# Kernel tuning notes

Hardware: AMD Instinct MI355X
Metric: run time of the kernel (lower is better)

The kernel has to match this reference:

```python
import jax, jax.numpy as jnp
import numpy as np

B, N, K, H = 8, 256, 64, 768
NUM_CLASSES = 10
D_SIM = 0.3  # self.d in the torch module


def setup_inputs() -> dict:
    key = jax.random.key(0)
    ks = jax.random.split(key, 12)
    s = 0.02  # init scale to keep 3 stacked linear GCN layers numerically tame
    return {
        "encoder_out": jax.random.normal(ks[0], (B, N, H), jnp.float32),
        "landmarks": jax.random.normal(ks[1], (K, H), jnp.float32),
        "alpha": jnp.array([0.5], jnp.float32),
        "gcn_w1": jax.random.normal(ks[2], (H, H), jnp.float32) * s,
        "gcn_b1": jnp.zeros((H,), jnp.float32),
        "gcn_w2": jax.random.normal(ks[3], (H, H), jnp.float32) * s,
        "gcn_b2": jnp.zeros((H,), jnp.float32),
        "gcn_w3": jax.random.normal(ks[4], (H, H), jnp.float32) * s,
        "gcn_b3": jnp.zeros((H,), jnp.float32),
        "fc1_w": jax.random.normal(ks[5], (1000, K * H), jnp.float32) * s,
        "fc1_b": jnp.zeros((1000,), jnp.float32),
        "fc2_w": jax.random.normal(ks[6], (100, 1000), jnp.float32) * s,
        "fc2_b": jnp.zeros((100,), jnp.float32),
        "fc3_w": jax.random.normal(ks[7], (NUM_CLASSES, 100), jnp.float32) * s,
        "fc3_b": jnp.zeros((NUM_CLASSES,), jnp.float32),
    }


def reference(encoder_out, landmarks, alpha,
              gcn_w1, gcn_b1, gcn_w2, gcn_b2, gcn_w3, gcn_b3,
              fc1_w, fc1_b, fc2_w, fc2_b, fc3_w, fc3_b):
    b, n, h = encoder_out.shape
    k = landmarks.shape[0]

    # distance_matrix: [B,N,K], min-max normalized over clusters
    diff = encoder_out[:, :, None, :] - landmarks[None, None, :, :]  # [B,N,K,H]
    dist = jnp.sqrt(jnp.sum(diff * diff, axis=-1))                   # [B,N,K]
    mn = dist.min(axis=-1, keepdims=True)
    mx = dist.max(axis=-1, keepdims=True)
    nd = (dist - mn) / (mx - mn + 1e-6)

    # probability_matrix: gaussian similarity, row-normalized
    sim = jnp.exp(-nd * nd / (2.0 * D_SIM * D_SIM))
    prob = sim / sim.sum(axis=-1, keepdims=True)  # [B,N,K]

    # compute_distance_weight: [N,N] smooth matrix
    idx = jnp.arange(n)
    dw = jnp.exp(-alpha[0] * jnp.abs(idx[:, None] - idx[None, :]).astype(jnp.float32))

    # graph_constructing: einsum('bik,bjl->bijkl') * W then sum over (k,l)
    # == bilinear form P @ W @ P^T, computed WITHOUT the 5-D tensor
    P = prob.transpose(0, 2, 1)                      # [B,K,N]
    G = jnp.einsum('bik,kl,bjl->bij', P, dw, P)      # [B,K,K]

    # cluster pooling: prob^T @ encoder_out -> [B,K,H]
    out = jnp.einsum('bnk,bnh->bkh', prob, encoder_out)
    out_ori = out  # dropout is identity at inference

    # gcn_batched: PyG GCNConv x3 on the dense graph G!=0, batched.
    # gcn_norm: add remaining self-loops, A_hat = A + I_missing,
    # out = D^-1/2 A_hat D^-1/2 (X W^T) + bias  (no nonlinearity between layers)
    A = (G != 0).astype(jnp.float32)                 # [B,K,K]
    A = jnp.maximum(A, jnp.eye(k, dtype=jnp.float32))
    deg = A.sum(axis=-1)                             # [B,K]
    dinv = jnp.where(deg > 0, 1.0 / jnp.sqrt(deg), 0.0)
    An = A * dinv[:, :, None] * dinv[:, None, :]     # normalized adjacency

    hx = out
    for w, bias in ((gcn_w1, gcn_b1), (gcn_w2, gcn_b2), (gcn_w3, gcn_b3)):
        hx = jnp.einsum('bij,bjh->bih', An, hx @ w.T) + bias
    gcn_out = hx + out  # residual inside gcn_batched

    x = (out_ori + gcn_out).reshape(b, -1)           # [B, K*H]
    x = jax.nn.gelu(x @ fc1_w.T + fc1_b, approximate=False)
    x = jax.nn.gelu(x @ fc2_w.T + fc2_b, approximate=False)
    return x @ fc3_w.T + fc3_b                       # [B, NUM_CLASSES]
```

## Files before the change

### kernel.cpp

```cpp
#include <hip/hip_runtime.h>
#include <math.h>

#define DEV __device__ __forceinline__

DEV float dot4(float4 a, float4 b){ return a.x*b.x + a.y*b.y + a.z*b.z + a.w*b.w; }

DEV float wave_sum(float v){
  #pragma unroll
  for (int off = 32; off; off >>= 1) v += __shfl_xor(v, off, 64);
  return v;
}

DEV float gelu_exact(float v){ return 0.5f * v * (1.f + erff(v * 0.70710678118654752f)); }

__global__ void k_lmT(const float* __restrict__ lm, float* __restrict__ lmT4,
                      float* __restrict__ lnorm){
  int k = blockIdx.x, t = threadIdx.x;
  __shared__ float red[256];
  float s = 0.f;
  if (t < 192){
    float4 v = *(const float4*)(lm + k*768 + 4*t);
    ((float4*)lmT4)[t*64 + k] = v;
    s = dot4(v, v);
  }
  red[t] = s; __syncthreads();
  for (int off = 128; off; off >>= 1){ if (t < off) red[t] += red[t+off]; __syncthreads(); }
  if (t == 0) lnorm[k] = red[0];
}

__global__ void k_prob(const float* __restrict__ enc, const float* __restrict__ lmT4,
                       const float* __restrict__ lnorm, float* __restrict__ prob){
  int t = threadIdx.x, lane = t & 63, wv = t >> 6;
  int row0 = blockIdx.x*8 + wv*2;
  const float4* LT = (const float4*)lmT4;
  const float4* X0 = (const float4*)(enc + (size_t)row0*768);
  const float4* X1 = (const float4*)(enc + (size_t)(row0+1)*768);
  float dot0=0.f, dot1=0.f, xn0=0.f, xn1=0.f;
  #pragma unroll 8
  for (int hg = 0; hg < 192; ++hg){
    float4 l4 = LT[hg*64 + lane];
    float4 a = X0[hg], b = X1[hg];
    dot0 += dot4(a, l4); dot1 += dot4(b, l4);
    xn0  += dot4(a, a);  xn1  += dot4(b, b);
  }
  float ln = lnorm[lane];
  float d0 = sqrtf(fmaxf(xn0 + ln - 2.f*dot0, 0.f));
  float d1 = sqrtf(fmaxf(xn1 + ln - 2.f*dot1, 0.f));
  float mn0=d0, mx0=d0, mn1=d1, mx1=d1;
  #pragma unroll
  for (int off = 32; off; off >>= 1){
    mn0 = fminf(mn0, __shfl_xor(mn0, off, 64));
    mx0 = fmaxf(mx0, __shfl_xor(mx0, off, 64));
    mn1 = fminf(mn1, __shfl_xor(mn1, off, 64));
    mx1 = fmaxf(mx1, __shfl_xor(mx1, off, 64));
  }
  float nd0 = (d0 - mn0) / (mx0 - mn0 + 1e-6f);
  float nd1 = (d1 - mn1) / (mx1 - mn1 + 1e-6f);
  float s0 = expf(nd0*nd0 * (-1.f/0.18f));
  float s1 = expf(nd1*nd1 * (-1.f/0.18f));
  float sum0 = wave_sum(s0), sum1 = wave_sum(s1);
  prob[(size_t)row0*64 + lane]     = s0 / sum0;
  prob[(size_t)(row0+1)*64 + lane] = s1 / sum1;
}

__global__ void k_pool(const float* __restrict__ enc, const float* __restrict__ prob,
                       float* __restrict__ outp, float* __restrict__ mbar){
  int b = blockIdx.x / 48, ch = blockIdx.x % 48;
  int lane = threadIdx.x & 63, wv = threadIdx.x >> 6;
  int h0 = ch*16 + wv*4;
  const float* E = enc + (size_t)b*256*768 + h0;
  const float* P = prob + (size_t)b*256*64;
  float acc[4] = {0,0,0,0};
  #pragma unroll 4
  for (int n = 0; n < 256; ++n){
    float p = P[n*64 + lane];
    float4 e0 = *(const float4*)(E + (size_t)n*768);
    acc[0] += p*e0.x; acc[1] += p*e0.y; acc[2] += p*e0.z; acc[3] += p*e0.w;
  }
  float* O = outp + ((size_t)b*64 + lane)*768 + h0;
  *(float4*)O = make_float4(acc[0],acc[1],acc[2],acc[3]);
  #pragma unroll
  for (int j = 0; j < 4; ++j){
    float v = wave_sum(acc[j]);
    if (lane == 0) mbar[(size_t)b*768 + h0 + j] = v * (1.f/64.f);
  }
}

__global__ void k_vm768(const float* __restrict__ in, const float* __restrict__ W,
                        const float* __restrict__ bias, float* __restrict__ out){
  int lane = threadIdx.x & 63, wv = threadIdx.x >> 6;
  int j = blockIdx.x*4 + wv;
  const float4* Wr = (const float4*)(W + (size_t)j*768);
  const float4* IN = (const float4*)in;
  float acc[8] = {0,0,0,0,0,0,0,0};
  #pragma unroll
  for (int s = 0; s < 3; ++s){
    int ig = s*64 + lane;
    float4 w4 = Wr[ig];
    #pragma unroll
    for (int b = 0; b < 8; ++b) acc[b] += dot4(w4, IN[b*192 + ig]);
  }
  #pragma unroll
  for (int b = 0; b < 8; ++b){
    float v = wave_sum(acc[b]);
    if (lane == 0) out[b*768 + j] = v + bias[j];
  }
}

__global__ void k_xcat(const float* __restrict__ outp, const float* __restrict__ hx3,
                       float* __restrict__ x){
  int idx = blockIdx.x*256 + threadIdx.x;
  int h4 = idx % 192;
  int b  = idx / (192*64);
  float4 o = ((const float4*)outp)[idx];
  float4 g = ((const float4*)hx3)[b*192 + h4];
  float4 r;
  r.x = 2.f*o.x + g.x; r.y = 2.f*o.y + g.y; r.z = 2.f*o.z + g.z; r.w = 2.f*o.w + g.w;
  ((float4*)x)[idx] = r;
}

__global__ void __launch_bounds__(256) k_fc1s(const float* __restrict__ x,
                                              const float* __restrict__ W,
                                              float* __restrict__ part_out){
  int t = threadIdx.x, lane = t & 63, wv = t >> 6;
  int kc = blockIdx.x / 125, jg = blockIdx.x % 125;
  int j0 = jg*8;
  const float4* Xg = (const float4*)x + kc*384;
  const float4* Wa = (const float4*)W + (size_t)(j0 + wv*2)*12288 + kc*384;
  const float4* Wb = Wa + 12288;
  __shared__ float4 xs4[3072];
  __shared__ float sp[64];

  float4 wa[6], wb[6];
  #pragma unroll
  for (int s = 0; s < 6; ++s){ wa[s] = Wa[s*64 + lane]; wb[s] = Wb[s*64 + lane]; }

  #pragma unroll
  for (int i = 0; i < 12; ++i){
    int idx = i*256 + t;
    int b = idx / 384, r = idx - b*384;
    xs4[idx] = Xg[b*12288 + r];
  }
  __syncthreads();

  float acc0[8] = {0,0,0,0,0,0,0,0};
  float acc1[8] = {0,0,0,0,0,0,0,0};
  #pragma unroll
  for (int s = 0; s < 6; ++s){
    int ig = s*64 + lane;
    #pragma unroll
    for (int b = 0; b < 8; ++b){
      float4 xv = xs4[b*384 + ig];
      acc0[b] += dot4(wa[s], xv);
      acc1[b] += dot4(wb[s], xv);
    }
  }

  #pragma unroll
  for (int b = 0; b < 8; ++b){
    float v0 = wave_sum(acc0[b]);
    float v1 = wave_sum(acc1[b]);
    if (lane == 0){ sp[(wv*2+0)*8 + b] = v0; sp[(wv*2+1)*8 + b] = v1; }
  }
  __syncthreads();
  if (t < 64)
    part_out[(size_t)kc*8000 + (size_t)j0*8 + t] = sp[t];
}

__global__ void k_fc1red(const float* __restrict__ part, const float* __restrict__ bias,
                         float* __restrict__ x1){
  int idx = blockIdx.x*256 + threadIdx.x;
  if (idx < 8000){
    int j = idx % 1000, b = idx / 1000;
    float v = 0.f;
    #pragma unroll
    for (int kc = 0; kc < 32; ++kc)
      v += part[kc*8000 + j*8 + b];
    x1[idx] = gelu_exact(v + bias[j]);
  }
}

__global__ void k_fc2(const float* __restrict__ x1, const float* __restrict__ W,
                      const float* __restrict__ bias, float* __restrict__ x2){
  int lane = threadIdx.x & 63, wv = threadIdx.x >> 6;
  int m = blockIdx.x*4 + wv;
  const float4* Wr = (const float4*)(W + (size_t)m*1000);
  const float4* X  = (const float4*)x1;
  float acc[8] = {0,0,0,0,0,0,0,0};
  for (int s = 0; s < 4; ++s){
    int jg = s*64 + lane;
    if (jg < 250){
      float4 w4 = Wr[jg];
      #pragma unroll
      for (int b = 0; b < 8; ++b) acc[b] += dot4(w4, X[b*250 + jg]);
    }
  }
  #pragma unroll
  for (int b = 0; b < 8; ++b){
    float v = wave_sum(acc[b]);
    if (lane == 0) x2[b*100 + m] = gelu_exact(v + bias[m]);
  }
}

__global__ void k_fc3(const float* __restrict__ x2, const float* __restrict__ W,
                      const float* __restrict__ bias, float* __restrict__ out){
  int t = threadIdx.x;
  if (t < 80){
    int b = t/10, c = t%10;
    float acc = bias[c];
    for (int m = 0; m < 100; ++m) acc += x2[b*100+m] * W[c*100+m];
    out[t] = acc;
  }
}

extern "C" void kernel_launch(void* const* d_in, const int* in_sizes, int n_in,
                              void* d_out, int out_size, void* d_ws, size_t ws_size,
                              hipStream_t stream){
  const float* enc = (const float*)d_in[0];
  const float* lm  = (const float*)d_in[1];
  const float* w1  = (const float*)d_in[3];
  const float* b1  = (const float*)d_in[4];
  const float* w2  = (const float*)d_in[5];
  const float* b2  = (const float*)d_in[6];
  const float* w3  = (const float*)d_in[7];
  const float* b3  = (const float*)d_in[8];
  const float* fw1 = (const float*)d_in[9];
  const float* fb1 = (const float*)d_in[10];
  const float* fw2 = (const float*)d_in[11];
  const float* fb2 = (const float*)d_in[12];
  const float* fw3 = (const float*)d_in[13];
  const float* fb3 = (const float*)d_in[14];

  float* ws    = (float*)d_ws;
  float* lmT4  = ws;
  float* lnorm = lmT4  + 49152;
  float* prob  = lnorm + 64;
  float* outp  = prob  + 131072;
  float* mbar  = outp  + 393216;
  float* hx1   = mbar  + 6144;
  float* hx2   = hx1   + 6144;
  float* hx3   = hx2   + 6144;
  float* xcat  = hx3   + 6144;
  float* fc1p  = xcat  + 393216;
  float* x1    = fc1p  + 256000;
  float* x2    = x1    + 8000;
  float* out   = (float*)d_out;

  k_lmT   <<<64,  256, 0, stream>>>(lm, lmT4, lnorm);
  k_prob  <<<256, 256, 0, stream>>>(enc, lmT4, lnorm, prob);
  k_pool  <<<384, 256, 0, stream>>>(enc, prob, outp, mbar);
  k_vm768 <<<192, 256, 0, stream>>>(mbar, w1, b1, hx1);
  k_vm768 <<<192, 256, 0, stream>>>(hx1,  w2, b2, hx2);
  k_vm768 <<<192, 256, 0, stream>>>(hx2,  w3, b3, hx3);
  k_xcat  <<<384, 256, 0, stream>>>(outp, hx3, xcat);
  k_fc1s  <<<4000,256, 0, stream>>>(xcat, fw1, fc1p);
  k_fc1red<<<32,  256, 0, stream>>>(fc1p, fb1, x1);
  k_fc2   <<<25,  256, 0, stream>>>(x1, fw2, fb2, x2);
  k_fc3   <<<1,   128, 0, stream>>>(x2, fw3, fb3, out);
}
```

Baseline: 144.6 us.

## Fuse landmark transpose, xcat, fc1 reduction and FC tail into fewer kernels

The landmark transpose and norm kernel is folded into k_prob, which now stages landmark chunks in shared memory and accumulates landmark norms in place. The xcat kernel is fused into the fc1 split-K kernel, which now uses half the K chunk and twice the blocks and reduces partials with atomicAdd into a buffer zeroed by k_prob. The fc1 reduction, fc2 and fc3 are merged into a single per-batch tail kernel. This removes several launches and the intermediate xcat and partial buffers, at the cost of atomic contention, redundant landmark norm work, and a nondeterministic summation order.

```diff
diff --git a/kernel.cpp b/kernel.cpp
--- a/kernel.cpp
+++ b/kernel.cpp
@@ -13,37 +13,37 @@
 
 DEV float gelu_exact(float v){ return 0.5f * v * (1.f + erff(v * 0.70710678118654752f)); }
 
-__global__ void k_lmT(const float* __restrict__ lm, float* __restrict__ lmT4,
-                      float* __restrict__ lnorm){
-  int k = blockIdx.x, t = threadIdx.x;
-  __shared__ float red[256];
-  float s = 0.f;
-  if (t < 192){
-    float4 v = *(const float4*)(lm + k*768 + 4*t);
-    ((float4*)lmT4)[t*64 + k] = v;
-    s = dot4(v, v);
-  }
-  red[t] = s; __syncthreads();
-  for (int off = 128; off; off >>= 1){ if (t < off) red[t] += red[t+off]; __syncthreads(); }
-  if (t == 0) lnorm[k] = red[0];
-}
-
-__global__ void k_prob(const float* __restrict__ enc, const float* __restrict__ lmT4,
-                       const float* __restrict__ lnorm, float* __restrict__ prob){
+__global__ void __launch_bounds__(256) k_prob(const float* __restrict__ lm,
+                                              const float* __restrict__ enc,
+                                              float* __restrict__ prob,
+                                              float* __restrict__ y1zero){
   int t = threadIdx.x, lane = t & 63, wv = t >> 6;
+  int gid = blockIdx.x*256 + t;
+  if (gid < 8000) y1zero[gid] = 0.f;
   int row0 = blockIdx.x*8 + wv*2;
-  const float4* LT = (const float4*)lmT4;
+  __shared__ float4 ls[3072];
+  const float4* L4 = (const float4*)lm;
   const float4* X0 = (const float4*)(enc + (size_t)row0*768);
-  const float4* X1 = (const float4*)(enc + (size_t)(row0+1)*768);
-  float dot0=0.f, dot1=0.f, xn0=0.f, xn1=0.f;
-  #pragma unroll 8
-  for (int hg = 0; hg < 192; ++hg){
-    float4 l4 = LT[hg*64 + lane];
-    float4 a = X0[hg], b = X1[hg];
-    dot0 += dot4(a, l4); dot1 += dot4(b, l4);
-    xn0  += dot4(a, a);  xn1  += dot4(b, b);
-  }
-  float ln = lnorm[lane];
+  const float4* X1 = X0 + 192;
+  float dot0=0.f, dot1=0.f, xn0=0.f, xn1=0.f, ln=0.f;
+  for (int c = 0; c < 4; ++c){
+    if (c) __syncthreads();
+    #pragma unroll
+    for (int i = 0; i < 12; ++i){
+      int idx = i*256 + t;
+      int k = idx & 63, col = idx >> 6;
+      ls[idx] = L4[k*192 + c*48 + col];
+    }
+    __syncthreads();
+    #pragma unroll 8
+    for (int hg = 0; hg < 48; ++hg){
+      float4 l4 = ls[hg*64 + lane];
+      float4 a = X0[c*48 + hg], b = X1[c*48 + hg];
+      dot0 += dot4(a, l4); dot1 += dot4(b, l4);
+      xn0  += dot4(a, a);  xn1  += dot4(b, b);
+      ln   += dot4(l4, l4);
+    }
+  }
   float d0 = sqrtf(fmaxf(xn0 + ln - 2.f*dot0, 0.f));
   float d1 = sqrtf(fmaxf(xn1 + ln - 2.f*dot1, 0.f));
   float mn0=d0, mx0=d0, mn1=d1, mx1=d1;
@@ -107,50 +107,44 @@
   }
 }
 
-__global__ void k_xcat(const float* __restrict__ outp, const float* __restrict__ hx3,
-                       float* __restrict__ x){
-  int idx = blockIdx.x*256 + threadIdx.x;
-  int h4 = idx % 192;
-  int b  = idx / (192*64);
-  float4 o = ((const float4*)outp)[idx];
-  float4 g = ((const float4*)hx3)[b*192 + h4];
-  float4 r;
-  r.x = 2.f*o.x + g.x; r.y = 2.f*o.y + g.y; r.z = 2.f*o.z + g.z; r.w = 2.f*o.w + g.w;
-  ((float4*)x)[idx] = r;
-}
-
-__global__ void __launch_bounds__(256) k_fc1s(const float* __restrict__ x,
+__global__ void __launch_bounds__(256) k_fc1s(const float* __restrict__ outp,
+                                              const float* __restrict__ hx3,
                                               const float* __restrict__ W,
-                                              float* __restrict__ part_out){
+                                              float* __restrict__ y1){
   int t = threadIdx.x, lane = t & 63, wv = t >> 6;
   int kc = blockIdx.x / 125, jg = blockIdx.x % 125;
   int j0 = jg*8;
-  const float4* Xg = (const float4*)x + kc*384;
-  const float4* Wa = (const float4*)W + (size_t)(j0 + wv*2)*12288 + kc*384;
+  const float4* O4 = (const float4*)outp + kc*192;
+  const float4* H4 = (const float4*)hx3;
+  const float4* Wa = (const float4*)W + (size_t)(j0 + wv*2)*12288 + kc*192;
   const float4* Wb = Wa + 12288;
-  __shared__ float4 xs4[3072];
+  __shared__ float4 xs4[1536];
   __shared__ float sp[64];
 
-  float4 wa[6], wb[6];
-  #pragma unroll
-  for (int s = 0; s < 6; ++s){ wa[s] = Wa[s*64 + lane]; wb[s] = Wb[s*64 + lane]; }
-
-  #pragma unroll
-  for (int i = 0; i < 12; ++i){
+  float4 wa[3], wb[3];
+  #pragma unroll
+  for (int s = 0; s < 3; ++s){ wa[s] = Wa[s*64 + lane]; wb[s] = Wb[s*64 + lane]; }
+
+  #pragma unroll
+  for (int i = 0; i < 6; ++i){
     int idx = i*256 + t;
-    int b = idx / 384, r = idx - b*384;
-    xs4[idx] = Xg[b*12288 + r];
+    int b = idx / 192, r = idx - b*192;
+    float4 o = O4[(size_t)b*12288 + r];
+    float4 g = H4[b*192 + r];
+    float4 v;
+    v.x = 2.f*o.x + g.x; v.y = 2.f*o.y + g.y; v.z = 2.f*o.z + g.z; v.w = 2.f*o.w + g.w;
+    xs4[idx] = v;
   }
   __syncthreads();
 
   float acc0[8] = {0,0,0,0,0,0,0,0};
   float acc1[8] = {0,0,0,0,0,0,0,0};
   #pragma unroll
-  for (int s = 0; s < 6; ++s){
+  for (int s = 0; s < 3; ++s){
     int ig = s*64 + lane;
     #pragma unroll
     for (int b = 0; b < 8; ++b){
-      float4 xv = xs4[b*384 + ig];
+      float4 xv = xs4[b*192 + ig];
       acc0[b] += dot4(wa[s], xv);
       acc1[b] += dot4(wb[s], xv);
     }
@@ -163,53 +157,48 @@
     if (lane == 0){ sp[(wv*2+0)*8 + b] = v0; sp[(wv*2+1)*8 + b] = v1; }
   }
   __syncthreads();
-  if (t < 64)
-    part_out[(size_t)kc*8000 + (size_t)j0*8 + t] = sp[t];
-}
-
-__global__ void k_fc1red(const float* __restrict__ part, const float* __restrict__ bias,
-                         float* __restrict__ x1){
-  int idx = blockIdx.x*256 + threadIdx.x;
-  if (idx < 8000){
-    int j = idx % 1000, b = idx / 1000;
-    float v = 0.f;
-    #pragma unroll
-    for (int kc = 0; kc < 32; ++kc)
-      v += part[kc*8000 + j*8 + b];
-    x1[idx] = gelu_exact(v + bias[j]);
-  }
-}
-
-__global__ void k_fc2(const float* __restrict__ x1, const float* __restrict__ W,
-                      const float* __restrict__ bias, float* __restrict__ x2){
-  int lane = threadIdx.x & 63, wv = threadIdx.x >> 6;
-  int m = blockIdx.x*4 + wv;
-  const float4* Wr = (const float4*)(W + (size_t)m*1000);
-  const float4* X  = (const float4*)x1;
-  float acc[8] = {0,0,0,0,0,0,0,0};
-  for (int s = 0; s < 4; ++s){
-    int jg = s*64 + lane;
-    if (jg < 250){
-      float4 w4 = Wr[jg];
-      #pragma unroll
-      for (int b = 0; b < 8; ++b) acc[b] += dot4(w4, X[b*250 + jg]);
-    }
-  }
-  #pragma unroll
-  for (int b = 0; b < 8; ++b){
-    float v = wave_sum(acc[b]);
-    if (lane == 0) x2[b*100 + m] = gelu_exact(v + bias[m]);
-  }
-}
-
-__global__ void k_fc3(const float* __restrict__ x2, const float* __restrict__ W,
-                      const float* __restrict__ bias, float* __restrict__ out){
-  int t = threadIdx.x;
-  if (t < 80){
-    int b = t/10, c = t%10;
-    float acc = bias[c];
-    for (int m = 0; m < 100; ++m) acc += x2[b*100+m] * W[c*100+m];
-    out[t] = acc;
+  if (t < 64){
+    int jp = t >> 3, b = t & 7;
+    atomicAdd(&y1[b*1000 + j0 + jp], sp[t]);
+  }
+}
+
+__global__ void __launch_bounds__(256) k_tail(const float* __restrict__ y1,
+                                              const float* __restrict__ fb1,
+                                              const float* __restrict__ W2,
+                                              const float* __restrict__ fb2,
+                                              const float* __restrict__ W3,
+                                              const float* __restrict__ fb3,
+                                              float* __restrict__ out){
+  int b = blockIdx.x, t = threadIdx.x, lane = t & 63, wv = t >> 6;
+  __shared__ __align__(16) float x1s[1000];
+  __shared__ float x2s[100];
+  #pragma unroll
+  for (int i = 0; i < 4; ++i){
+    int j = i*256 + t;
+    if (j < 1000) x1s[j] = gelu_exact(y1[b*1000 + j] + fb1[j]);
+  }
+  __syncthreads();
+  const float4* X4 = (const float4*)x1s;
+  for (int i = 0; i < 25; ++i){
+    int m = wv*25 + i;
+    const float4* Wr = (const float4*)(W2 + (size_t)m*1000);
+    float acc = 0.f;
+    #pragma unroll
+    for (int s = 0; s < 4; ++s){
+      int jg = s*64 + lane;
+      if (jg < 250) acc += dot4(Wr[jg], X4[jg]);
+    }
+    acc = wave_sum(acc);
+    if (lane == 0) x2s[m] = gelu_exact(acc + fb2[m]);
+  }
+  __syncthreads();
+  if (t < 10){
+    float acc = fb3[t];
+    const float* Wr = W3 + t*100;
+    #pragma unroll 4
+    for (int m = 0; m < 100; ++m) acc += x2s[m]*Wr[m];
+    out[b*10 + t] = acc;
   }
 }
 
@@ -232,29 +221,20 @@
   const float* fb3 = (const float*)d_in[14];
 
   float* ws    = (float*)d_ws;
-  float* lmT4  = ws;
-  float* lnorm = lmT4  + 49152;
-  float* prob  = lnorm + 64;
+  float* prob  = ws;
   float* outp  = prob  + 131072;
   float* mbar  = outp  + 393216;
   float* hx1   = mbar  + 6144;
   float* hx2   = hx1   + 6144;
   float* hx3   = hx2   + 6144;
-  float* xcat  = hx3   + 6144;
-  float* fc1p  = xcat  + 393216;
-  float* x1    = fc1p  + 256000;
-  float* x2    = x1    + 8000;
+  float* y1raw = hx3   + 6144;
   float* out   = (float*)d_out;
 
-  k_lmT   <<<64,  256, 0, stream>>>(lm, lmT4, lnorm);
-  k_prob  <<<256, 256, 0, stream>>>(enc, lmT4, lnorm, prob);
-  k_pool  <<<384, 256, 0, stream>>>(enc, prob, outp, mbar);
-  k_vm768 <<<192, 256, 0, stream>>>(mbar, w1, b1, hx1);
-  k_vm768 <<<192, 256, 0, stream>>>(hx1,  w2, b2, hx2);
-  k_vm768 <<<192, 256, 0, stream>>>(hx2,  w3, b3, hx3);
-  k_xcat  <<<384, 256, 0, stream>>>(outp, hx3, xcat);
-  k_fc1s  <<<4000,256, 0, stream>>>(xcat, fw1, fc1p);
-  k_fc1red<<<32,  256, 0, stream>>>(fc1p, fb1, x1);
-  k_fc2   <<<25,  256, 0, stream>>>(x1, fw2, fb2, x2);
-  k_fc3   <<<1,   128, 0, stream>>>(x2, fw3, fb3, out);
-}
+  k_prob <<<256, 256, 0, stream>>>(lm, enc, prob, y1raw);
+  k_pool <<<384, 256, 0, stream>>>(enc, prob, outp, mbar);
+  k_vm768<<<192, 256, 0, stream>>>(mbar, w1, b1, hx1);
+  k_vm768<<<192, 256, 0, stream>>>(hx1,  w2, b2, hx2);
+  k_vm768<<<192, 256, 0, stream>>>(hx2,  w3, b3, hx3);
+  k_fc1s <<<8000,256, 0, stream>>>(outp, hx3, fw1, y1raw);
+  k_tail <<<8,   256, 0, stream>>>(y1raw, fb1, fw2, fb2, fw3, fb3, out);
+}
```

Result: slower. 158.8 us (+9.8%).
